# Performance work log

Measured on AMD Instinct MI355X. Metric: run time of the kernel, lower is better.

The kernel has to match this reference:

```python
import jax, jax.numpy as jnp
import numpy as np
from jax import lax

KSIZE = 7
SIGMA = 5.0
ALPHA = 0.05


def _gaussian_kernel(ksize: int, sigma: float) -> jnp.ndarray:
    # 2D Gaussian, normalized to sum 1, replicated depthwise for 3 channels: (3,1,k,k)
    ax = jnp.arange(ksize, dtype=jnp.float32) - (ksize - 1) / 2.0
    g1 = jnp.exp(-(ax ** 2) / (2.0 * sigma ** 2))
    g2 = jnp.outer(g1, g1)
    g2 = g2 / jnp.sum(g2)
    return jnp.broadcast_to(g2[None, None], (3, 1, ksize, ksize)).astype(jnp.float32)


def _sobel_kernel() -> jnp.ndarray:
    # (2,1,3,3): channel 0 -> Ix, channel 1 -> Iy
    sx = jnp.array([[-1.0, 0.0, 1.0], [-2.0, 0.0, 2.0], [-1.0, 0.0, 1.0]], dtype=jnp.float32)
    sy = sx.T
    return jnp.stack([sx[None], sy[None]], axis=0)  # (2,1,3,3)


def setup_inputs() -> dict:
    key = jax.random.key(0)
    x = jax.random.normal(key, (1, 1, 4096, 4096), dtype=jnp.float32)
    return {"x": x, "sobel_k": _sobel_kernel(), "gauss_k": _gaussian_kernel(KSIZE, SIGMA)}


def _conv(x, k, pad, groups):
    return lax.conv_general_dilated(
        x, k, window_strides=(1, 1), padding=[(pad, pad), (pad, pad)],
        dimension_numbers=("NCHW", "OIHW", "NCHW"), feature_group_count=groups)


def reference(x, sobel_k, gauss_k):
    # ImageGradientsLayer: Sobel conv -> (1,2,H,W)
    g = _conv(x, sobel_k, 1, 1)
    Ix, Iy = g[:, 0:1], g[:, 1:2]
    # ChannelProductLayer -> (1,3,H,W)
    prod = jnp.concatenate([Ix * Ix, Iy * Iy, Ix * Iy], axis=1)
    # SecondMomentMatrixLayer: depthwise Gaussian blur, groups=3
    S = _conv(prod, gauss_k, KSIZE // 2, 3)
    Sxx, Syy, Sxy = S[0, 0], S[0, 1], S[0, 2]
    # CornerResponseLayer: R = det - alpha*trace^2
    tr = Sxx + Syy
    R = (Sxx * Syy - Sxy * Sxy - ALPHA * tr * tr)[None, None]  # (1,1,H,W)
    # NMSLayer: median threshold, 7x7 maxpool (stride 1, pad 3), keep maxima
    med = jnp.median(R)
    Rt = jnp.where(R >= med, R, jnp.float32(0.0))
    mp = lax.reduce_window(Rt, -jnp.inf, lax.max, (1, 1, 7, 7), (1, 1, 1, 1),
                           [(0, 0), (0, 0), (3, 3), (3, 3)])
    out = jnp.where(Rt != mp, jnp.float32(0.0), mp)
    return out
```

## Files before the change

### kernel.cpp

```cpp
#include <hip/hip_runtime.h>
#include <math.h>

#define N_IMG 4096
#define NBC   1024
#define H_OUT 32
#define HR    38
#define NPIX  (N_IMG * N_IMG)

struct W7 { float w[7]; };

__device__ __forceinline__ unsigned f2k(float f) {
    unsigned u = __float_as_uint(f);
    return (u & 0x80000000u) ? ~u : (u | 0x80000000u);
}
__device__ __forceinline__ float k2f(unsigned k) {
    unsigned u = (k & 0x80000000u) ? (k & 0x7fffffffu) : ~k;
    return __uint_as_float(u);
}

struct SelState { unsigned p1, p2, r1, r2; };

template<int BINS>
__device__ void locate_pair(const unsigned* __restrict__ h0,
                            const unsigned* __restrict__ h1,
                            int shift, SelState& s)
{
    __shared__ unsigned scan[256];
    __shared__ unsigned resb[2], resr[2];
    const int tid = threadIdx.x;
    const int per = BINS / 256;
    const bool same = (h0 == h1);

    for (int q = 0; q < 2; q++) {
        if (q == 1 && same) break;
        const unsigned* __restrict__ h = q ? h1 : h0;
        const int base = tid * per;
        unsigned sum = 0;
        #pragma unroll
        for (int i = 0; i < per; i++) sum += h[base + i];
        __syncthreads();
        scan[tid] = sum;
        __syncthreads();
        unsigned v = sum;
        #pragma unroll
        for (int off = 1; off < 256; off <<= 1) {
            unsigned t = (tid >= off) ? scan[tid - off] : 0u;
            __syncthreads();
            v += t;
            scan[tid] = v;
            __syncthreads();
        }
        const unsigned excl = v - sum;
        #pragma unroll
        for (int w = 0; w < 2; w++) {
            const unsigned rank = w ? s.r2 : s.r1;
            const bool mine = w ? (same || q == 1) : (q == 0);
            if (mine && rank >= excl && rank < v) {
                unsigned rr = rank - excl;
                for (int i = 0; i < per; i++) {
                    unsigned c = h[base + i];
                    if (rr < c) { resb[w] = (unsigned)(base + i); resr[w] = rr; break; }
                    rr -= c;
                }
            }
        }
        __syncthreads();
    }
    s.p1 |= resb[0] << shift; s.r1 = resr[0];
    s.p2 |= resb[1] << shift; s.r2 = resr[1];
}

__device__ __forceinline__ SelState derive0(const unsigned* __restrict__ g0) {
    SelState s; s.p1 = 0u; s.p2 = 0u;
    s.r1 = (unsigned)(NPIX / 2 - 1); s.r2 = (unsigned)(NPIX / 2);
    locate_pair<4096>(g0, g0, 20, s);
    return s;
}
__device__ __forceinline__ void derive1(const unsigned* __restrict__ g1, SelState& s) {
    const unsigned* h1 = (s.p1 != s.p2) ? (g1 + 4096) : g1;
    locate_pair<4096>(g1, h1, 8, s);
}
__device__ __forceinline__ void derive2(const unsigned* __restrict__ g2, SelState& s) {
    const unsigned* h1 = (s.p1 != s.p2) ? (g2 + 256) : g2;
    locate_pair<256>(g2, h1, 0, s);
}

__global__ __launch_bounds__(256, 2) void harris_kernel(const float* __restrict__ x,
                                                        float* __restrict__ R,
                                                        unsigned* __restrict__ g0,
                                                        W7 wp)
{
    __shared__ unsigned histo[4096];
    const int tid = threadIdx.x;
    for (int i = tid; i < 4096; i += 256) histo[i] = 0;
    __syncthreads();

    const int row0 = blockIdx.y * H_OUT;
    const int jc   = blockIdx.x * NBC + tid * 4;
    const float* w = wp.w;

    float xm[12], xc[12], xp[12];
    float hxx[7][4], hyy[7][4], hxy[7][4];

    auto loadrow = [&](int ri, float* d) {
        if ((unsigned)ri < N_IMG) {
            const float* p = x + (size_t)ri * N_IMG;
            float4 v0 = make_float4(0.f,0.f,0.f,0.f), v2 = make_float4(0.f,0.f,0.f,0.f);
            if (jc >= 4) v0 = *(const float4*)(p + jc - 4);
            float4 v1 = *(const float4*)(p + jc);
            if (jc + 4 < N_IMG) v2 = *(const float4*)(p + jc + 4);
            d[0]=v0.x; d[1]=v0.y; d[2]=v0.z; d[3]=v0.w;
            d[4]=v1.x; d[5]=v1.y; d[6]=v1.z; d[7]=v1.w;
            d[8]=v2.x; d[9]=v2.y; d[10]=v2.z; d[11]=v2.w;
        } else {
            #pragma unroll
            for (int t = 0; t < 12; t++) d[t] = 0.f;
        }
    };

    loadrow(row0 - 4, xm);
    loadrow(row0 - 3, xc);

    int curb = -1; unsigned cnt = 0;

    for (int it = 0; it < 6; ++it) {
        #pragma unroll
        for (int k = 0; k < 7; ++k) {
            const int r = it * 7 + k;
            if (r < HR) {
                const int ri = row0 + r - 3;
                loadrow(ri + 1, xp);

                float sxx[4] = {0,0,0,0}, syy[4] = {0,0,0,0}, sxy[4] = {0,0,0,0};
                if ((unsigned)ri < N_IMG) {
                    float dc[12], rd[12];
                    #pragma unroll
                    for (int t = 0; t < 12; t++) {
                        dc[t] = xm[t] + 2.f * xc[t] + xp[t];
                        rd[t] = xp[t] - xm[t];
                    }
                    #pragma unroll
                    for (int t = 0; t < 10; t++) {
                        float ix = dc[t+2] - dc[t];
                        float iy = rd[t] + 2.f * rd[t+1] + rd[t+2];
                        if ((unsigned)(jc - 3 + t) >= N_IMG) { ix = 0.f; iy = 0.f; }
                        float xx = ix*ix, yy = iy*iy, xy = ix*iy;
                        #pragma unroll
                        for (int o = 0; o < 4; o++) {
                            int v = t - o;
                            if (v >= 0 && v < 7) {
                                sxx[o] = fmaf(w[v], xx, sxx[o]);
                                syy[o] = fmaf(w[v], yy, syy[o]);
                                sxy[o] = fmaf(w[v], xy, sxy[o]);
                            }
                        }
                    }
                }
                #pragma unroll
                for (int o = 0; o < 4; o++) {
                    hxx[k][o] = sxx[o]; hyy[k][o] = syy[o]; hxy[k][o] = sxy[o];
                }

                if (r >= 6) {
                    float4 h;
                    float* hp = &h.x;
                    #pragma unroll
                    for (int o = 0; o < 4; o++) {
                        float ax = 0.f, ay = 0.f, az = 0.f;
                        #pragma unroll
                        for (int u = 0; u < 7; u++) {
                            const int s = (k + 1 + u) % 7;
                            ax = fmaf(w[u], hxx[s][o], ax);
                            ay = fmaf(w[u], hyy[s][o], ay);
                            az = fmaf(w[u], hxy[s][o], az);
                        }
                        float tr = ax + ay;
                        hp[o] = ax*ay - az*az - 0.05f*tr*tr;
                    }
                    const int orow = row0 + r - 6;
                    *(float4*)(R + (size_t)orow * N_IMG + jc) = h;
                    #pragma unroll
                    for (int o = 0; o < 4; o++) {
                        int b = (int)(f2k(hp[o]) >> 20);
                        if (b == curb) cnt++;
                        else { if (curb >= 0) atomicAdd(&histo[curb], cnt); curb = b; cnt = 1; }
                    }
                }
                #pragma unroll
                for (int t = 0; t < 12; t++) { xm[t] = xc[t]; xc[t] = xp[t]; }
            }
        }
    }
    if (curb >= 0) atomicAdd(&histo[curb], cnt);
    __syncthreads();
    for (int i = tid; i < 4096; i += 256) {
        unsigned c = histo[i];
        if (c) atomicAdd(&g0[i], c);
    }
}

__global__ __launch_bounds__(256) void hist1_kernel(const float* __restrict__ R,
                                                    const unsigned* __restrict__ g0,
                                                    unsigned* __restrict__ g1)
{
    __shared__ unsigned h[2][4096];
    const int tid = threadIdx.x;
    for (int i = tid; i < 8192; i += 256) ((unsigned*)h)[i] = 0u;

    SelState s = derive0(g0);
    const unsigned p1 = s.p1, p2 = s.p2;
    const bool dual = (p1 != p2);
    const unsigned mask = 0xFFF00000u;
    const int shift = 8;

    const int n4 = NPIX / 4;
    int curb1 = -1; unsigned cnt1 = 0;
    int curb2 = -1; unsigned cnt2 = 0;
    const float4* R4 = (const float4*)R;
    for (int i = blockIdx.x * 256 + tid; i < n4; i += gridDim.x * 256) {
        float4 v = R4[i];
        float vv[4] = {v.x, v.y, v.z, v.w};
        #pragma unroll
        for (int t = 0; t < 4; t++) {
            unsigned k = f2k(vv[t]);
            if ((k & mask) == p1) {
                int b = (int)((k >> shift) & 4095u);
                if (b == curb1) cnt1++;
                else { if (cnt1) atomicAdd(&h[0][curb1], cnt1); curb1 = b; cnt1 = 1; }
            }
            if (dual && (k & mask) == p2) {
                int b = (int)((k >> shift) & 4095u);
                if (b == curb2) cnt2++;
                else { if (cnt2) atomicAdd(&h[1][curb2], cnt2); curb2 = b; cnt2 = 1; }
            }
        }
    }
    if (cnt1) atomicAdd(&h[0][curb1], cnt1);
    if (cnt2) atomicAdd(&h[1][curb2], cnt2);
    __syncthreads();
    for (int i = tid; i < 4096; i += 256) {
        unsigned c0 = h[0][i]; if (c0) atomicAdd(&g1[i], c0);
        if (dual) { unsigned c1 = h[1][i]; if (c1) atomicAdd(&g1[4096 + i], c1); }
    }
}

__global__ __launch_bounds__(256) void hist2_kernel(const float* __restrict__ R,
                                                    const unsigned* __restrict__ g0,
                                                    const unsigned* __restrict__ g1,
                                                    unsigned* __restrict__ g2)
{
    __shared__ unsigned h[2][256];
    const int tid = threadIdx.x;
    for (int i = tid; i < 512; i += 256) ((unsigned*)h)[i] = 0u;

    SelState s = derive0(g0);
    derive1(g1, s);
    const unsigned p1 = s.p1, p2 = s.p2;
    const bool dual = (p1 != p2);
    const unsigned mask = 0xFFFFFF00u;

    const int n4 = NPIX / 4;
    int curb1 = -1; unsigned cnt1 = 0;
    int curb2 = -1; unsigned cnt2 = 0;
    const float4* R4 = (const float4*)R;
    for (int i = blockIdx.x * 256 + tid; i < n4; i += gridDim.x * 256) {
        float4 v = R4[i];
        float vv[4] = {v.x, v.y, v.z, v.w};
        #pragma unroll
        for (int t = 0; t < 4; t++) {
            unsigned k = f2k(vv[t]);
            if ((k & mask) == p1) {
                int b = (int)(k & 255u);
                if (b == curb1) cnt1++;
                else { if (cnt1) atomicAdd(&h[0][curb1], cnt1); curb1 = b; cnt1 = 1; }
            }
            if (dual && (k & mask) == p2) {
                int b = (int)(k & 255u);
                if (b == curb2) cnt2++;
                else { if (cnt2) atomicAdd(&h[1][curb2], cnt2); curb2 = b; cnt2 = 1; }
            }
        }
    }
    if (cnt1) atomicAdd(&h[0][curb1], cnt1);
    if (cnt2) atomicAdd(&h[1][curb2], cnt2);
    __syncthreads();
    if (tid < 256) {
        unsigned c0 = h[0][tid]; if (c0) atomicAdd(&g2[tid], c0);
        if (dual) { unsigned c1 = h[1][tid]; if (c1) atomicAdd(&g2[256 + tid], c1); }
    }
}

__global__ __launch_bounds__(256) void init_kernel(unsigned* __restrict__ g)
{
    const int tid = threadIdx.x;
    for (int i = tid; i < 16384; i += 256) g[i] = 0u;
}

__global__ __launch_bounds__(256, 2) void nms_kernel(const float* __restrict__ R,
                                                     const unsigned* __restrict__ g0,
                                                     const unsigned* __restrict__ g1,
                                                     const unsigned* __restrict__ g2,
                                                     float* __restrict__ out)
{
    const int tid  = threadIdx.x;

    SelState s = derive0(g0);
    derive1(g1, s);
    derive2(g2, s);
    const float med = 0.5f * (k2f(s.p1) + k2f(s.p2));

    const int row0 = blockIdx.y * H_OUT;
    const int jc   = blockIdx.x * NBC + tid * 4;

    float hm[7][4], ct[7][4];

    for (int it = 0; it < 6; ++it) {
        #pragma unroll
        for (int k = 0; k < 7; ++k) {
            const int r = it * 7 + k;
            if (r < HR) {
                const int ri = row0 + r - 3;
                float a[12];
                if ((unsigned)ri < N_IMG) {
                    const float* p = R + (size_t)ri * N_IMG;
                    float4 v1 = *(const float4*)(p + jc);
                    a[4] = (v1.x >= med) ? v1.x : 0.f;
                    a[5] = (v1.y >= med) ? v1.y : 0.f;
                    a[6] = (v1.z >= med) ? v1.z : 0.f;
                    a[7] = (v1.w >= med) ? v1.w : 0.f;
                    if (jc >= 4) {
                        float4 v0 = *(const float4*)(p + jc - 4);
                        a[0] = (v0.x >= med) ? v0.x : 0.f;
                        a[1] = (v0.y >= med) ? v0.y : 0.f;
                        a[2] = (v0.z >= med) ? v0.z : 0.f;
                        a[3] = (v0.w >= med) ? v0.w : 0.f;
                    } else { a[0]=a[1]=a[2]=a[3] = -INFINITY; }
                    if (jc + 4 < N_IMG) {
                        float4 v2 = *(const float4*)(p + jc + 4);
                        a[8]  = (v2.x >= med) ? v2.x : 0.f;
                        a[9]  = (v2.y >= med) ? v2.y : 0.f;
                        a[10] = (v2.z >= med) ? v2.z : 0.f;
                        a[11] = (v2.w >= med) ? v2.w : 0.f;
                    } else { a[8]=a[9]=a[10]=a[11] = -INFINITY; }
                } else {
                    #pragma unroll
                    for (int t = 0; t < 12; t++) a[t] = -INFINITY;
                }
                #pragma unroll
                for (int o = 0; o < 4; o++) {
                    float m = a[o+1];
                    #pragma unroll
                    for (int t = 2; t <= 7; t++) m = fmaxf(m, a[o+t]);
                    hm[k][o] = m;
                    ct[k][o] = a[4+o];
                }
                if (r >= 6) {
                    float4 ov;
                    float* op = &ov.x;
                    #pragma unroll
                    for (int o = 0; o < 4; o++) {
                        float m = hm[(k+1) % 7][o];
                        #pragma unroll
                        for (int u = 1; u < 7; u++) m = fmaxf(m, hm[(k+1+u) % 7][o]);
                        float c = ct[(k+4) % 7][o];
                        op[o] = (c != m) ? 0.f : m;
                    }
                    const int orow = row0 + r - 6;
                    *(float4*)(out + (size_t)orow * N_IMG + jc) = ov;
                }
            }
        }
    }
}

extern "C" void kernel_launch(void* const* d_in, const int* in_sizes, int n_in,
                              void* d_out, int out_size, void* d_ws, size_t ws_size,
                              hipStream_t stream)
{
    const float* x = (const float*)d_in[0];
    float* R = (float*)d_ws;
    unsigned* g0 = (unsigned*)((char*)d_ws + (size_t)N_IMG * N_IMG * 4);
    unsigned* g1 = g0 + 4096;
    unsigned* g2 = g1 + 8192;
    float* out = (float*)d_out;

    W7 wp;
    {
        double g[7], sm = 0.0;
        for (int i = 0; i < 7; i++) { double ax = (double)i - 3.0; g[i] = exp(-(ax*ax)/50.0); sm += g[i]; }
        for (int i = 0; i < 7; i++) wp.w[i] = (float)(g[i] / sm);
    }

    dim3 sgrid(N_IMG / NBC, N_IMG / H_OUT);

    init_kernel<<<1, 256, 0, stream>>>(g0);
    harris_kernel<<<sgrid, 256, 0, stream>>>(x, R, g0, wp);
    hist1_kernel<<<2048, 256, 0, stream>>>(R, g0, g1);
    hist2_kernel<<<2048, 256, 0, stream>>>(R, g0, g1, g2);
    nms_kernel<<<sgrid, 256, 0, stream>>>(R, g0, g1, g2, out);
}
```

Baseline: 295.2 us.

## Switch vertical blur and max-pool to scatter-accumulate rings, peel warmup rows

The vertical 7-tap Gaussian in harris_kernel and the vertical 7-row max in nms_kernel used to gather from a ring of stored horizontal results at every output row. They now scatter-accumulate each new horizontal result into seven rolling accumulators and emit and reset one accumulator per row. The first seven rows are peeled so their loop bounds are compile-time constants, and the column boundary masking in the Sobel step only runs for edge threads. The total arithmetic stays about the same. The aim is to reduce per-row dependency chains and branches, at the cost of a different summation order and roughly the same register footprint.

```diff
diff --git a/kernel.cpp b/kernel.cpp
--- a/kernel.cpp
+++ b/kernel.cpp
@@ -98,9 +98,15 @@
     const int row0 = blockIdx.y * H_OUT;
     const int jc   = blockIdx.x * NBC + tid * 4;
     const float* w = wp.w;
+    const bool edge = (jc < 4) || (jc >= N_IMG - 8);
 
     float xm[12], xc[12], xp[12];
-    float hxx[7][4], hyy[7][4], hxy[7][4];
+    float axx[7][4], ayy[7][4], axy[7][4];
+
+    #pragma unroll
+    for (int m = 0; m < 7; m++)
+        #pragma unroll
+        for (int o = 0; o < 4; o++) { axx[m][o] = 0.f; ayy[m][o] = 0.f; axy[m][o] = 0.f; }
 
     auto loadrow = [&](int ri, float* d) {
         if ((unsigned)ri < N_IMG) {
@@ -123,74 +129,91 @@
 
     int curb = -1; unsigned cnt = 0;
 
-    for (int it = 0; it < 6; ++it) {
+    auto step = [&](int r, int k, int dmin, bool emit) {
+        const int ri = row0 + r - 3;
+        loadrow(ri + 1, xp);
+
+        if ((unsigned)ri < N_IMG) {
+            float dc[12], rd[12];
+            #pragma unroll
+            for (int t = 0; t < 12; t++) {
+                dc[t] = xm[t] + 2.f * xc[t] + xp[t];
+                rd[t] = xp[t] - xm[t];
+            }
+            float ixv[10], iyv[10];
+            #pragma unroll
+            for (int t = 0; t < 10; t++) {
+                ixv[t] = dc[t+2] - dc[t];
+                iyv[t] = rd[t] + 2.f * rd[t+1] + rd[t+2];
+            }
+            if (edge) {
+                #pragma unroll
+                for (int t = 0; t < 10; t++)
+                    if ((unsigned)(jc - 3 + t) >= N_IMG) { ixv[t] = 0.f; iyv[t] = 0.f; }
+            }
+            float sxx[4] = {0,0,0,0}, syy[4] = {0,0,0,0}, sxy[4] = {0,0,0,0};
+            #pragma unroll
+            for (int t = 0; t < 10; t++) {
+                float ix = ixv[t], iy = iyv[t];
+                float xx = ix*ix, yy = iy*iy, xy = ix*iy;
+                #pragma unroll
+                for (int o = 0; o < 4; o++) {
+                    const int v = t - o;
+                    if (v >= 0 && v < 7) {
+                        sxx[o] = fmaf(w[v], xx, sxx[o]);
+                        syy[o] = fmaf(w[v], yy, syy[o]);
+                        sxy[o] = fmaf(w[v], xy, sxy[o]);
+                    }
+                }
+            }
+            #pragma unroll
+            for (int d = 0; d < 7; d++) {
+                if (d >= dmin) {
+                    const int m = (k + d) % 7;
+                    #pragma unroll
+                    for (int o = 0; o < 4; o++) {
+                        axx[m][o] = fmaf(w[6-d], sxx[o], axx[m][o]);
+                        ayy[m][o] = fmaf(w[6-d], syy[o], ayy[m][o]);
+                        axy[m][o] = fmaf(w[6-d], sxy[o], axy[m][o]);
+                    }
+                }
+            }
+        }
+
+        if (emit) {
+            float4 h;
+            float* hp = &h.x;
+            #pragma unroll
+            for (int o = 0; o < 4; o++) {
+                float ax = axx[k][o], ay = ayy[k][o], az = axy[k][o];
+                axx[k][o] = 0.f; ayy[k][o] = 0.f; axy[k][o] = 0.f;
+                float tr = ax + ay;
+                hp[o] = ax*ay - az*az - 0.05f*tr*tr;
+            }
+            const int orow = row0 + r - 6;
+            *(float4*)(R + (size_t)orow * N_IMG + jc) = h;
+            #pragma unroll
+            for (int o = 0; o < 4; o++) {
+                int b = (int)(f2k(hp[o]) >> 20);
+                if (b == curb) cnt++;
+                else { if (curb >= 0) atomicAdd(&histo[curb], cnt); curb = b; cnt = 1; }
+            }
+        }
+        #pragma unroll
+        for (int t = 0; t < 12; t++) { xm[t] = xc[t]; xc[t] = xp[t]; }
+    };
+
+    #pragma unroll
+    for (int rr = 0; rr < 7; ++rr)
+        step(rr, rr, 6 - rr, rr == 6);
+    for (int it = 1; it < 6; ++it) {
         #pragma unroll
         for (int k = 0; k < 7; ++k) {
             const int r = it * 7 + k;
-            if (r < HR) {
-                const int ri = row0 + r - 3;
-                loadrow(ri + 1, xp);
-
-                float sxx[4] = {0,0,0,0}, syy[4] = {0,0,0,0}, sxy[4] = {0,0,0,0};
-                if ((unsigned)ri < N_IMG) {
-                    float dc[12], rd[12];
-                    #pragma unroll
-                    for (int t = 0; t < 12; t++) {
-                        dc[t] = xm[t] + 2.f * xc[t] + xp[t];
-                        rd[t] = xp[t] - xm[t];
-                    }
-                    #pragma unroll
-                    for (int t = 0; t < 10; t++) {
-                        float ix = dc[t+2] - dc[t];
-                        float iy = rd[t] + 2.f * rd[t+1] + rd[t+2];
-                        if ((unsigned)(jc - 3 + t) >= N_IMG) { ix = 0.f; iy = 0.f; }
-                        float xx = ix*ix, yy = iy*iy, xy = ix*iy;
-                        #pragma unroll
-                        for (int o = 0; o < 4; o++) {
-                            int v = t - o;
-                            if (v >= 0 && v < 7) {
-                                sxx[o] = fmaf(w[v], xx, sxx[o]);
-                                syy[o] = fmaf(w[v], yy, syy[o]);
-                                sxy[o] = fmaf(w[v], xy, sxy[o]);
-                            }
-                        }
-                    }
-                }
-                #pragma unroll
-                for (int o = 0; o < 4; o++) {
-                    hxx[k][o] = sxx[o]; hyy[k][o] = syy[o]; hxy[k][o] = sxy[o];
-                }
-
-                if (r >= 6) {
-                    float4 h;
-                    float* hp = &h.x;
-                    #pragma unroll
-                    for (int o = 0; o < 4; o++) {
-                        float ax = 0.f, ay = 0.f, az = 0.f;
-                        #pragma unroll
-                        for (int u = 0; u < 7; u++) {
-                            const int s = (k + 1 + u) % 7;
-                            ax = fmaf(w[u], hxx[s][o], ax);
-                            ay = fmaf(w[u], hyy[s][o], ay);
-                            az = fmaf(w[u], hxy[s][o], az);
-                        }
-                        float tr = ax + ay;
-                        hp[o] = ax*ay - az*az - 0.05f*tr*tr;
-                    }
-                    const int orow = row0 + r - 6;
-                    *(float4*)(R + (size_t)orow * N_IMG + jc) = h;
-                    #pragma unroll
-                    for (int o = 0; o < 4; o++) {
-                        int b = (int)(f2k(hp[o]) >> 20);
-                        if (b == curb) cnt++;
-                        else { if (curb >= 0) atomicAdd(&histo[curb], cnt); curb = b; cnt = 1; }
-                    }
-                }
-                #pragma unroll
-                for (int t = 0; t < 12; t++) { xm[t] = xc[t]; xc[t] = xp[t]; }
-            }
-        }
-    }
+            if (r < HR) step(r, k, 0, true);
+        }
+    }
+
     if (curb >= 0) atomicAdd(&histo[curb], cnt);
     __syncthreads();
     for (int i = tid; i < 4096; i += 256) {
@@ -312,63 +335,86 @@
     const int row0 = blockIdx.y * H_OUT;
     const int jc   = blockIdx.x * NBC + tid * 4;
 
-    float hm[7][4], ct[7][4];
-
-    for (int it = 0; it < 6; ++it) {
+    float vm[7][4];
+    float ct[7][4];
+    #pragma unroll
+    for (int m = 0; m < 7; m++)
+        #pragma unroll
+        for (int o = 0; o < 4; o++) vm[m][o] = -INFINITY;
+
+    auto loadrowT = [&](int ri, float* d) {
+        if ((unsigned)ri < N_IMG) {
+            const float* p = R + (size_t)ri * N_IMG;
+            float4 v1 = *(const float4*)(p + jc);
+            d[4] = (v1.x >= med) ? v1.x : 0.f;
+            d[5] = (v1.y >= med) ? v1.y : 0.f;
+            d[6] = (v1.z >= med) ? v1.z : 0.f;
+            d[7] = (v1.w >= med) ? v1.w : 0.f;
+            if (jc >= 4) {
+                float4 v0 = *(const float4*)(p + jc - 4);
+                d[0] = (v0.x >= med) ? v0.x : 0.f;
+                d[1] = (v0.y >= med) ? v0.y : 0.f;
+                d[2] = (v0.z >= med) ? v0.z : 0.f;
+                d[3] = (v0.w >= med) ? v0.w : 0.f;
+            } else { d[0]=d[1]=d[2]=d[3] = -INFINITY; }
+            if (jc + 4 < N_IMG) {
+                float4 v2 = *(const float4*)(p + jc + 4);
+                d[8]  = (v2.x >= med) ? v2.x : 0.f;
+                d[9]  = (v2.y >= med) ? v2.y : 0.f;
+                d[10] = (v2.z >= med) ? v2.z : 0.f;
+                d[11] = (v2.w >= med) ? v2.w : 0.f;
+            } else { d[8]=d[9]=d[10]=d[11] = -INFINITY; }
+        } else {
+            #pragma unroll
+            for (int t = 0; t < 12; t++) d[t] = -INFINITY;
+        }
+    };
+
+    auto stepn = [&](int r, int k, int dmin, bool emit) {
+        const int ri = row0 + r - 3;
+        float a[12];
+        loadrowT(ri, a);
+        float hm[4];
+        #pragma unroll
+        for (int o = 0; o < 4; o++) {
+            float m01 = fmaxf(a[o+1], a[o+2]);
+            float m23 = fmaxf(a[o+3], a[o+4]);
+            float m45 = fmaxf(a[o+5], a[o+6]);
+            hm[o] = fmaxf(fmaxf(m01, m23), fmaxf(m45, a[o+7]));
+            ct[k][o] = a[4+o];
+        }
+        #pragma unroll
+        for (int d = 0; d < 7; d++) {
+            if (d >= dmin) {
+                const int m = (k + d) % 7;
+                #pragma unroll
+                for (int o = 0; o < 4; o++)
+                    vm[m][o] = fmaxf(vm[m][o], hm[o]);
+            }
+        }
+        if (emit) {
+            float4 ov;
+            float* op = &ov.x;
+            #pragma unroll
+            for (int o = 0; o < 4; o++) {
+                float m = vm[k][o];
+                vm[k][o] = -INFINITY;
+                float c = ct[(k+4) % 7][o];
+                op[o] = (c != m) ? 0.f : m;
+            }
+            const int orow = row0 + r - 6;
+            *(float4*)(out + (size_t)orow * N_IMG + jc) = ov;
+        }
+    };
+
+    #pragma unroll
+    for (int rr = 0; rr < 7; ++rr)
+        stepn(rr, rr, 6 - rr, rr == 6);
+    for (int it = 1; it < 6; ++it) {
         #pragma unroll
         for (int k = 0; k < 7; ++k) {
             const int r = it * 7 + k;
-            if (r < HR) {
-                const int ri = row0 + r - 3;
-                float a[12];
-                if ((unsigned)ri < N_IMG) {
-                    const float* p = R + (size_t)ri * N_IMG;
-                    float4 v1 = *(const float4*)(p + jc);
-                    a[4] = (v1.x >= med) ? v1.x : 0.f;
-                    a[5] = (v1.y >= med) ? v1.y : 0.f;
-                    a[6] = (v1.z >= med) ? v1.z : 0.f;
-                    a[7] = (v1.w >= med) ? v1.w : 0.f;
-                    if (jc >= 4) {
-                        float4 v0 = *(const float4*)(p + jc - 4);
-                        a[0] = (v0.x >= med) ? v0.x : 0.f;
-                        a[1] = (v0.y >= med) ? v0.y : 0.f;
-                        a[2] = (v0.z >= med) ? v0.z : 0.f;
-                        a[3] = (v0.w >= med) ? v0.w : 0.f;
-                    } else { a[0]=a[1]=a[2]=a[3] = -INFINITY; }
-                    if (jc + 4 < N_IMG) {
-                        float4 v2 = *(const float4*)(p + jc + 4);
-                        a[8]  = (v2.x >= med) ? v2.x : 0.f;
-                        a[9]  = (v2.y >= med) ? v2.y : 0.f;
-                        a[10] = (v2.z >= med) ? v2.z : 0.f;
-                        a[11] = (v2.w >= med) ? v2.w : 0.f;
-                    } else { a[8]=a[9]=a[10]=a[11] = -INFINITY; }
-                } else {
-                    #pragma unroll
-                    for (int t = 0; t < 12; t++) a[t] = -INFINITY;
-                }
-                #pragma unroll
-                for (int o = 0; o < 4; o++) {
-                    float m = a[o+1];
-                    #pragma unroll
-                    for (int t = 2; t <= 7; t++) m = fmaxf(m, a[o+t]);
-                    hm[k][o] = m;
-                    ct[k][o] = a[4+o];
-                }
-                if (r >= 6) {
-                    float4 ov;
-                    float* op = &ov.x;
-                    #pragma unroll
-                    for (int o = 0; o < 4; o++) {
-                        float m = hm[(k+1) % 7][o];
-                        #pragma unroll
-                        for (int u = 1; u < 7; u++) m = fmaxf(m, hm[(k+1+u) % 7][o]);
-                        float c = ct[(k+4) % 7][o];
-                        op[o] = (c != m) ? 0.f : m;
-                    }
-                    const int orow = row0 + r - 6;
-                    *(float4*)(out + (size_t)orow * N_IMG + jc) = ov;
-                }
-            }
+            if (r < HR) stepn(r, k, 0, true);
         }
     }
 }
```

Result: faster. 289.1 us (-2.1%).
